# Kernel tuning notes

Measured on AMD Instinct MI355X. Metric: run time of the kernel, lower is better.

## Reference

```python
import jax, jax.numpy as jnp
import numpy as np

B, N, D = 2, 2048, 1024
H = 16
HD = D // H
SCALE = HD ** -0.5


def setup_inputs() -> dict:
    key = jax.random.key(0)
    k1, k2, kw, kb = jax.random.split(key, 4)
    x1 = jax.random.normal(k1, (B, N, D), dtype=jnp.float32)
    x2 = jax.random.normal(k2, (B, N, D), dtype=jnp.float32)
    # fused qkv linear: torch nn.Linear(dim, 3*dim): W [3D, D], b [3D]
    bound = 1.0 / np.sqrt(D)
    qkv_w = jax.random.uniform(kw, (3 * D, D), minval=-bound, maxval=bound, dtype=jnp.float32)
    qkv_b = jax.random.uniform(kb, (3 * D,), minval=-bound, maxval=bound, dtype=jnp.float32)
    return {"x1": x1, "x2": x2, "qkv_w": qkv_w, "qkv_b": qkv_b}


def reference(x1, x2, qkv_w, qkv_b):
    # qkv projections (only q from x1 and k,v from x2 are used by the module)
    q1 = (jnp.einsum('bnd,ed->bne', x1, qkv_w[:D]) + qkv_b[:D])
    k2 = (jnp.einsum('bnd,ed->bne', x2, qkv_w[D:2 * D]) + qkv_b[D:2 * D])
    v2 = (jnp.einsum('bnd,ed->bne', x2, qkv_w[2 * D:]) + qkv_b[2 * D:])
    # [B, H, N, HD]
    q1 = q1.reshape(B, N, H, HD).transpose(0, 2, 1, 3)
    k2 = k2.reshape(B, N, H, HD).transpose(0, 2, 1, 3)
    v2 = v2.reshape(B, N, H, HD).transpose(0, 2, 1, 3)
    # explicit QK^T -> softmax -> AV (materializes [B,H,N,N] like the original)
    scores = jnp.einsum('bhqd,bhkd->bhqk', q1, k2) * SCALE
    attn = jax.nn.softmax(scores, axis=-1)
    out = jnp.einsum('bhqk,bhkd->bhqd', attn, v2)
    # [B, N, D]; note original module skips out_proj (never applied in forward)
    return out.transpose(0, 2, 1, 3).reshape(B, N, D)
```

## Files before the change

kernel.cpp:

```cpp
#include <hip/hip_runtime.h>
#include <cstdint>
#include <cstddef>

#define B_   2
#define N_   2048
#define D_   1024
#define H_   16
#define HD_  64
#define QSCALE_ 0.18033688011112042f

typedef unsigned short u16;
typedef unsigned int   u32;
typedef __attribute__((ext_vector_type(8))) short short8;
typedef __attribute__((ext_vector_type(4))) float f32x4;
typedef __attribute__((ext_vector_type(16))) float f32x16;
typedef __attribute__((ext_vector_type(4))) float fl4;
typedef __attribute__((ext_vector_type(4))) unsigned short us4;
typedef __attribute__((ext_vector_type(4))) unsigned int u32x4;

#if __has_builtin(__builtin_amdgcn_exp2f)
#define EXP2F(x) __builtin_amdgcn_exp2f(x)
#else
#define EXP2F(x) exp2f(x)
#endif

__device__ __forceinline__ u16 f2bf(float f) {
  u32 u = __builtin_bit_cast(u32, f);
  u += 0x7fffu + ((u >> 16) & 1u);
  return (u16)(u >> 16);
}

__device__ __forceinline__ u32 cvtpk(float lo, float hi) {
  u32 r;
  asm("v_cvt_pk_bf16_f32 %0, %1, %2" : "=v"(r) : "v"(lo), "v"(hi));
  return r;
}

__device__ __forceinline__ void plswap(u32& a, u32& b) {
  asm volatile("v_permlane32_swap_b32 %0, %1" : "+v"(a), "+v"(b));
}

__device__ __forceinline__ void gload16(const void* g, void* l) {
  typedef __attribute__((address_space(1))) unsigned int gu32;
  typedef __attribute__((address_space(3))) unsigned int lu32;
  __builtin_amdgcn_global_load_lds((gu32*)g, (lu32*)l, 16, 0, 0);
}

__global__ void convert_kernel(const fl4* __restrict__ x1, const fl4* __restrict__ x2,
                               const fl4* __restrict__ w,
                               us4* __restrict__ o1, us4* __restrict__ o2,
                               us4* __restrict__ ow) {
  const int NX = (B_ * N_ * D_) / 4;
  const int NW = (3 * D_ * D_) / 4;
  int stride = gridDim.x * blockDim.x;
  for (int i = blockIdx.x * blockDim.x + threadIdx.x; i < NX; i += stride) {
    fl4 a = x1[i];
    us4 r; r.x = f2bf(a.x); r.y = f2bf(a.y); r.z = f2bf(a.z); r.w = f2bf(a.w);
    o1[i] = r;
    fl4 b = x2[i];
    us4 s; s.x = f2bf(b.x); s.y = f2bf(b.y); s.z = f2bf(b.z); s.w = f2bf(b.w);
    o2[i] = s;
    if (i < NW) {
      fl4 c = w[i];
      us4 t; t.x = f2bf(c.x); t.y = f2bf(c.y); t.z = f2bf(c.z); t.w = f2bf(c.w);
      ow[i] = t;
    }
  }
}

__global__ __launch_bounds__(256) void qkv_gemm(
    const u16* __restrict__ x1b, const u16* __restrict__ x2b,
    const u16* __restrict__ wb, const float* __restrict__ bias,
    u16* __restrict__ Qb, u16* __restrict__ Kb, u16* __restrict__ Vtb) {
  const int z = blockIdx.z;
  const u16* X = (z == 0) ? x1b : x2b;
  const u16* W = wb + (size_t)z * D_ * D_;
  const float* bz = bias + z * D_;
  const int m0 = blockIdx.y * 128;
  const int e0 = blockIdx.x * 128;
  const int tid = threadIdx.x;
  const int lane = tid & 63;
  const int w = tid >> 6;
  const int wr = w >> 1, wc = w & 1;
  const int col = lane & 15, quad = lane >> 4;

  __shared__ __align__(16) u16 As[2][128 * 32];
  __shared__ __align__(16) u16 Bs[2][128 * 32];

  f32x4 acc[4][4] = {};

  int off0 = w * 2048 + lane * 16;
  int row0 = off0 >> 6;
  int ke0  = (off0 & 63) >> 1;
  int off1 = off0 + 1024;
  int row1 = off1 >> 6;
  int ke1  = (off1 & 63) >> 1;

  const u16* gA0 = X + (size_t)(m0 + row0) * D_ + ke0;
  const u16* gA1 = X + (size_t)(m0 + row1) * D_ + ke1;
  const u16* gB0 = W + (size_t)(e0 + row0) * D_ + ke0;
  const u16* gB1 = W + (size_t)(e0 + row1) * D_ + ke1;
  const int wbase = w * 1024;

#define STAGE(buf, k0)                                    \
  do {                                                    \
    gload16(gA0 + (k0), &As[buf][wbase]);                 \
    gload16(gA1 + (k0), &As[buf][wbase + 512]);           \
    gload16(gB0 + (k0), &Bs[buf][wbase]);                 \
    gload16(gB1 + (k0), &Bs[buf][wbase + 512]);           \
  } while (0)

  STAGE(0, 0);
  __syncthreads();

  for (int t = 0; t < D_ / 32; ++t) {
    const int cur = t & 1;
    if (t < D_ / 32 - 1) STAGE(cur ^ 1, (t + 1) * 32);

    short8 a[4], b[4];
#pragma unroll
    for (int i = 0; i < 4; ++i)
      a[i] = *(const short8*)&As[cur][(wr * 64 + i * 16 + col) * 32 + quad * 8];
#pragma unroll
    for (int j = 0; j < 4; ++j)
      b[j] = *(const short8*)&Bs[cur][(wc * 64 + j * 16 + col) * 32 + quad * 8];
    __builtin_amdgcn_s_setprio(1);
#pragma unroll
    for (int i = 0; i < 4; ++i)
#pragma unroll
      for (int j = 0; j < 4; ++j)
        acc[i][j] = __builtin_amdgcn_mfma_f32_16x16x32_bf16(a[i], b[j], acc[i][j], 0, 0, 0);
    __builtin_amdgcn_s_setprio(0);

    __syncthreads();
  }
#undef STAGE

#pragma unroll
  for (int j = 0; j < 4; ++j) {
    int eg = e0 + wc * 64 + j * 16 + col;
    float bj = bz[eg];
    int h = eg >> 6, d = eg & 63;
#pragma unroll
    for (int i = 0; i < 4; ++i) {
#pragma unroll
      for (int r = 0; r < 4; ++r) {
        int m = m0 + wr * 64 + i * 16 + quad * 4 + r;
        int bb = m >> 11, n = m & (N_ - 1);
        float v = acc[i][j][r] + bj;
        if (z == 0) v *= QSCALE_;
        u16 o = f2bf(v);
        if (z == 0)      Qb [(((size_t)bb * H_ + h) * N_ + n) * HD_ + d] = o;
        else if (z == 1) Kb [(((size_t)bb * H_ + h) * N_ + n) * HD_ + d] = o;
        else             Vtb[(((size_t)bb * H_ + h) * HD_ + d) * N_ + n] = o;
      }
    }
  }
}

__global__ __launch_bounds__(256, 2) void attn_kernel(
    const u16* __restrict__ Qb, const u16* __restrict__ Kb,
    const u16* __restrict__ Vtb, float* __restrict__ out) {
  const int bh = blockIdx.y;
  const int bb = bh >> 4, h = bh & 15;
  const int q0 = blockIdx.x * 128;
  const int tid = threadIdx.x;
  const int lane = tid & 63;
  const int w = tid >> 6;
  const int l31 = lane & 31, hf = lane >> 5, r7 = lane & 7;

  const u16* __restrict__ Q  = Qb  + ((size_t)bh << 17);
  const u16* __restrict__ K  = Kb  + ((size_t)bh << 17);
  const u16* __restrict__ Vt = Vtb + ((size_t)bh << 17);

  __shared__ __align__(16) u16 Ks[2][64 * 64];
  __shared__ __align__(16) u16 Vs[2][64 * 64];
  __shared__ float Ls[4][32];

  const u16* Qr = Q + (size_t)(q0 + w * 32 + l31) * HD_;
  short8 qf[4];
#pragma unroll
  for (int c = 0; c < 4; ++c)
    qf[c] = *(const short8*)&Qr[c * 16 + hf * 8];

  const int srow = tid >> 3;
  const int sg   = tid & 7;
  const int lw0 = srow * 64 + ((sg ^ (srow & 7)) * 8);
  const int lw1 = lw0 + 2048;
  const u16* gK = K + tid * 8;
  const u16* gV = Vt + srow * N_ + sg * 8;

  f32x16 accO[2] = {};
  float lsum = 0.f;

  short8 kA = *(const short8*)(gK);
  short8 kB = *(const short8*)(gK + 2048);
  short8 vA = *(const short8*)(gV);
  short8 vB = *(const short8*)(gV + 32 * N_);
  *(short8*)&Ks[0][lw0] = kA;
  *(short8*)&Ks[0][lw1] = kB;
  *(short8*)&Vs[0][lw0] = vA;
  *(short8*)&Vs[0][lw1] = vB;

  for (int t = 0; t < N_ / 64; ++t) {
    __syncthreads();
    const int cur = t & 1;
    if (t < N_ / 64 - 1) {
      const int k0n = (t + 1) * 64;
      kA = *(const short8*)(gK + k0n * 64);
      kB = *(const short8*)(gK + k0n * 64 + 2048);
      vA = *(const short8*)(gV + k0n);
      vB = *(const short8*)(gV + k0n + 32 * N_);
    }
    const u16* Kc = Ks[cur];
    const u16* Vc = Vs[cur];

    f32x16 sT[2] = {};
    __builtin_amdgcn_s_setprio(1);
#pragma unroll
    for (int kb = 0; kb < 2; ++kb) {
      const int rb = (kb * 32 + l31) * 64;
#pragma unroll
      for (int c = 0; c < 4; ++c) {
        short8 kf = *(const short8*)&Kc[rb + (((c * 2 + hf) ^ r7) * 8)];
        sT[kb] = __builtin_amdgcn_mfma_f32_32x32x16_bf16(kf, qf[c], sT[kb], 0, 0, 0);
      }
    }
    __builtin_amdgcn_s_setprio(0);

#pragma unroll
    for (int kb = 0; kb < 2; ++kb)
#pragma unroll
      for (int i = 0; i < 16; ++i) {
        float e = EXP2F(sT[kb][i]);
        lsum += e;
        sT[kb][i] = e;
      }

    short8 pf[4];
#pragma unroll
    for (int kc = 0; kc < 4; ++kc) {
      const int kb = kc >> 1, o = (kc & 1) * 8;
      u32 X = cvtpk(sT[kb][o + 0], sT[kb][o + 1]);
      u32 Y = cvtpk(sT[kb][o + 4], sT[kb][o + 5]);
      plswap(X, Y);
      u32 Z = cvtpk(sT[kb][o + 2], sT[kb][o + 3]);
      u32 W = cvtpk(sT[kb][o + 6], sT[kb][o + 7]);
      plswap(Z, W);
      u32x4 pw = {X, Z, Y, W};
      pf[kc] = __builtin_bit_cast(short8, pw);
    }

    __builtin_amdgcn_s_setprio(1);
#pragma unroll
    for (int db = 0; db < 2; ++db) {
      const int rb = (db * 32 + l31) * 64;
#pragma unroll
      for (int kc = 0; kc < 4; ++kc) {
        short8 vf = *(const short8*)&Vc[rb + (((kc * 2 + hf) ^ r7) * 8)];
        accO[db] = __builtin_amdgcn_mfma_f32_32x32x16_bf16(pf[kc], vf, accO[db], 0, 0, 0);
      }
    }
    __builtin_amdgcn_s_setprio(0);

    if (t < N_ / 64 - 1) {
      u16* Kn = (u16*)Ks[cur ^ 1];
      u16* Vn = (u16*)Vs[cur ^ 1];
      *(short8*)&Kn[lw0] = kA;
      *(short8*)&Kn[lw1] = kB;
      *(short8*)&Vn[lw0] = vA;
      *(short8*)&Vn[lw1] = vB;
    }
  }

  lsum += __shfl_xor(lsum, 32);
  if (hf == 0) Ls[w][l31] = 1.0f / lsum;
  __syncthreads();

  float rinv[16];
#pragma unroll
  for (int r = 0; r < 16; ++r)
    rinv[r] = Ls[w][(r & 3) + 8 * (r >> 2) + 4 * hf];

#pragma unroll
  for (int db = 0; db < 2; ++db)
#pragma unroll
    for (int r = 0; r < 16; ++r) {
      int n = q0 + w * 32 + (r & 3) + 8 * (r >> 2) + 4 * hf;
      int e = h * HD_ + db * 32 + l31;
      out[((size_t)bb * N_ + n) * D_ + e] = accO[db][r] * rinv[r];
    }
}

extern "C" void kernel_launch(void* const* d_in, const int* in_sizes, int n_in,
                              void* d_out, int out_size, void* d_ws, size_t ws_size,
                              hipStream_t stream) {
  const float* x1 = (const float*)d_in[0];
  const float* x2 = (const float*)d_in[1];
  const float* qw = (const float*)d_in[2];
  const float* qb = (const float*)d_in[3];
  float* out = (float*)d_out;

  u16* ws   = (u16*)d_ws;
  u16* x1b  = ws;
  u16* x2b  = ws + 4194304;
  u16* wb   = ws + 8388608;
  u16* Qbf  = ws + 11534336;
  u16* Kbf  = ws + 15728640;
  u16* Vtb  = ws + 19922944;
  if (ws_size < (size_t)24117248 * 2) return;

  convert_kernel<<<dim3(1024), dim3(256), 0, stream>>>(
      (const fl4*)x1, (const fl4*)x2, (const fl4*)qw,
      (us4*)x1b, (us4*)x2b, (us4*)wb);

  qkv_gemm<<<dim3(8, 32, 3), dim3(256), 0, stream>>>(
      x1b, x2b, wb, qb, Qbf, Kbf, Vtb);

  attn_kernel<<<dim3(16, 32), dim3(256), 0, stream>>>(Qbf, Kbf, Vtb, out);
}
```

Measured before the change: 178.0 us.

## Triple-buffer QKV GEMM loads with vmcnt waits and swizzle workgroups across XCDs

```diff
diff --git a/kernel.cpp b/kernel.cpp
--- a/kernel.cpp
+++ b/kernel.cpp
@@ -72,69 +72,86 @@
     const u16* __restrict__ x1b, const u16* __restrict__ x2b,
     const u16* __restrict__ wb, const float* __restrict__ bias,
     u16* __restrict__ Qb, u16* __restrict__ Kb, u16* __restrict__ Vtb) {
-  const int z = blockIdx.z;
+  const int wg  = blockIdx.x;
+  const int swz = (wg & 7) * 96 + (wg >> 3);
+  const int z   = swz >> 8;
+  const int e0  = ((swz >> 5) & 7) * 128;
+  const int m0  = (swz & 31) * 128;
+
   const u16* X = (z == 0) ? x1b : x2b;
   const u16* W = wb + (size_t)z * D_ * D_;
   const float* bz = bias + z * D_;
-  const int m0 = blockIdx.y * 128;
-  const int e0 = blockIdx.x * 128;
   const int tid = threadIdx.x;
   const int lane = tid & 63;
   const int w = tid >> 6;
   const int wr = w >> 1, wc = w & 1;
   const int col = lane & 15, quad = lane >> 4;
 
-  __shared__ __align__(16) u16 As[2][128 * 32];
-  __shared__ __align__(16) u16 Bs[2][128 * 32];
+  __shared__ __align__(16) u16 lds[3 * 8192];
 
   f32x4 acc[4][4] = {};
 
-  int off0 = w * 2048 + lane * 16;
-  int row0 = off0 >> 6;
-  int ke0  = (off0 & 63) >> 1;
-  int off1 = off0 + 1024;
-  int row1 = off1 >> 6;
-  int ke1  = (off1 & 63) >> 1;
-
-  const u16* gA0 = X + (size_t)(m0 + row0) * D_ + ke0;
-  const u16* gA1 = X + (size_t)(m0 + row1) * D_ + ke1;
-  const u16* gB0 = W + (size_t)(e0 + row0) * D_ + ke0;
-  const u16* gB1 = W + (size_t)(e0 + row1) * D_ + ke1;
-  const int wbase = w * 1024;
-
-#define STAGE(buf, k0)                                    \
+  const int srow = tid >> 2;
+  const int sseg = tid & 3;
+  const u16* srcA = X + (size_t)(m0 + srow) * D_ + sseg * 8;
+  const u16* srcB = W + (size_t)(e0 + srow) * D_ + sseg * 8;
+  u16* dA = &lds[w * 512];
+  u16* dB = &lds[4096 + w * 512];
+
+#define STAGE(uu, soff)                                   \
   do {                                                    \
-    gload16(gA0 + (k0), &As[buf][wbase]);                 \
-    gload16(gA1 + (k0), &As[buf][wbase + 512]);           \
-    gload16(gB0 + (k0), &Bs[buf][wbase]);                 \
-    gload16(gB1 + (k0), &Bs[buf][wbase + 512]);           \
+    const int kk0 = (uu) * 32;                            \
+    gload16(srcA + kk0,           dA + (soff));           \
+    gload16(srcA + 64 * D_ + kk0, dA + (soff) + 2048);    \
+    gload16(srcB + kk0,           dB + (soff));           \
+    gload16(srcB + 64 * D_ + kk0, dB + (soff) + 2048);    \
   } while (0)
 
+#define COMPUTE(roff)                                                        \
+  do {                                                                       \
+    const u16* Ar = &lds[(roff)];                                            \
+    const u16* Br = &lds[(roff) + 4096];                                     \
+    short8 a[4], b[4];                                                       \
+    _Pragma("unroll")                                                        \
+    for (int i = 0; i < 4; ++i)                                              \
+      a[i] = *(const short8*)&Ar[(wr * 64 + i * 16 + col) * 32 + quad * 8];  \
+    _Pragma("unroll")                                                        \
+    for (int j = 0; j < 4; ++j)                                              \
+      b[j] = *(const short8*)&Br[(wc * 64 + j * 16 + col) * 32 + quad * 8];  \
+    __builtin_amdgcn_s_setprio(1);                                           \
+    _Pragma("unroll")                                                        \
+    for (int i = 0; i < 4; ++i)                                              \
+      _Pragma("unroll")                                                      \
+      for (int j = 0; j < 4; ++j)                                            \
+        acc[i][j] = __builtin_amdgcn_mfma_f32_16x16x32_bf16(a[i], b[j],      \
+                                                            acc[i][j], 0, 0, 0); \
+    __builtin_amdgcn_s_setprio(0);                                           \
+  } while (0)
+
   STAGE(0, 0);
-  __syncthreads();
-
-  for (int t = 0; t < D_ / 32; ++t) {
-    const int cur = t & 1;
-    if (t < D_ / 32 - 1) STAGE(cur ^ 1, (t + 1) * 32);
-
-    short8 a[4], b[4];
-#pragma unroll
-    for (int i = 0; i < 4; ++i)
-      a[i] = *(const short8*)&As[cur][(wr * 64 + i * 16 + col) * 32 + quad * 8];
-#pragma unroll
-    for (int j = 0; j < 4; ++j)
-      b[j] = *(const short8*)&Bs[cur][(wc * 64 + j * 16 + col) * 32 + quad * 8];
-    __builtin_amdgcn_s_setprio(1);
-#pragma unroll
-    for (int i = 0; i < 4; ++i)
-#pragma unroll
-      for (int j = 0; j < 4; ++j)
-        acc[i][j] = __builtin_amdgcn_mfma_f32_16x16x32_bf16(a[i], b[j], acc[i][j], 0, 0, 0);
-    __builtin_amdgcn_s_setprio(0);
-
-    __syncthreads();
+  STAGE(1, 8192);
+  asm volatile("s_waitcnt vmcnt(4)" ::: "memory");
+  __builtin_amdgcn_s_barrier();
+  asm volatile("" ::: "memory");
+
+  int r_off = 0, s_off = 16384;
+  for (int u = 0; u < 30; ++u) {
+    STAGE(u + 2, s_off);
+    COMPUTE(r_off);
+    asm volatile("s_waitcnt vmcnt(4)" ::: "memory");
+    __builtin_amdgcn_s_barrier();
+    asm volatile("" ::: "memory");
+    r_off = (r_off == 16384) ? 0 : r_off + 8192;
+    s_off = (s_off == 16384) ? 0 : s_off + 8192;
   }
+  asm volatile("s_waitcnt vmcnt(0)" ::: "memory");
+  __builtin_amdgcn_s_barrier();
+  asm volatile("" ::: "memory");
+  COMPUTE(r_off);
+  r_off = (r_off == 16384) ? 0 : r_off + 8192;
+  COMPUTE(r_off);
 #undef STAGE
+#undef COMPUTE
 
 #pragma unroll
   for (int j = 0; j < 4; ++j) {
@@ -314,7 +331,7 @@
       (const fl4*)x1, (const fl4*)x2, (const fl4*)qw,
       (us4*)x1b, (us4*)x2b, (us4*)wb);
 
-  qkv_gemm<<<dim3(8, 32, 3), dim3(256), 0, stream>>>(
+  qkv_gemm<<<dim3(768), dim3(256), 0, stream>>>(
       x1b, x2b, wb, qb, Qbf, Kbf, Vtb);
 
   attn_kernel<<<dim3(16, 32), dim3(256), 0, stream>>>(Qbf, Kbf, Vtb, out);
```

Result: slower. 185.5 us (+4.2%).
